# Optimization experiments

Hardware: AMD Instinct MI355X
Metric: run time of the kernel (lower is better)

The kernel has to match this reference:

```python
import jax, jax.numpy as jnp
import numpy as np

D_MODEL = 1024
N_HEADS = 16

def setup_inputs() -> dict:
    key = jax.random.key(0)
    k1, k2, k3, k4 = jax.random.split(key, 4)
    B, L, S = 4, 2048, 2048
    return {
        "queries": jax.random.normal(k1, (B, L, D_MODEL), dtype=jnp.float32),
        "keys": jax.random.normal(k2, (B, S, D_MODEL), dtype=jnp.float32),
        "values": jax.random.normal(k3, (B, S, D_MODEL), dtype=jnp.float32),
        "mask": jax.random.uniform(k4, (L, S), dtype=jnp.float32),
    }

def reference(queries, keys, values, mask):
    B, L, _ = queries.shape
    S = keys.shape[1]
    H = N_HEADS
    q = queries.reshape(B, L, H, -1)  # (B,L,H,E)
    k = keys.reshape(B, S, H, -1)     # (B,S,H,E)
    v = values.reshape(B, S, H, -1)   # (B,S,H,D)
    E = q.shape[-1]
    scale = 1.0 / jnp.sqrt(jnp.asarray(E, q.dtype))
    scores = jnp.einsum('blhe,bshe->bhls', q, k)  # (B,H,L,S)
    A = jax.nn.softmax(scale * scores, axis=-1)
    # post-softmax multiplicative mask, broadcast over (B,H)
    A = A * mask
    out = jnp.einsum('bhls,bshd->blhd', A, v)  # (B,L,H,D)
    # mix=True: transpose(2,1) then flatten -> reshape (B,H,L,D) contiguously to (B,L,H*D)
    out = jnp.transpose(out, (0, 2, 1, 3)).reshape(B, L, -1)
    return out
```

## Files before the change

kernel.cpp:

```cpp
#include <hip/hip_runtime.h>
#include <hip/hip_bf16.h>

#define NH 16
#define LQ 2048
#define SK 2048
#define QTILE 128
#define KVB 32
#define NSBLK (SK / KVB)
#define TILE_BYTES 8192
#define MTILE_BYTES 8192
#define KV_BYTES ((size_t)4 * NH * NSBLK * TILE_BYTES)
#define MASK_OFF KV_BYTES
#define WS_NEED (KV_BYTES + (size_t)16 * NSBLK * MTILE_BYTES)
#define KSTR 72

typedef __bf16 bf16_t;
typedef bf16_t bf16x8 __attribute__((ext_vector_type(8)));
typedef bf16_t bf16x4 __attribute__((ext_vector_type(4)));
typedef bf16_t bf16x2 __attribute__((ext_vector_type(2)));
typedef float f32x16 __attribute__((ext_vector_type(16)));
typedef float f32x4 __attribute__((ext_vector_type(4)));
typedef unsigned int uint2v __attribute__((ext_vector_type(2)));
typedef unsigned int uint4v __attribute__((ext_vector_type(4)));

union U4B8 { uint4v u; bf16x8 v; };

__device__ __forceinline__ bf16x8 cvt8v(f32x4 a, f32x4 b) {
  bf16x8 r;
  r[0]=(bf16_t)a[0]; r[1]=(bf16_t)a[1]; r[2]=(bf16_t)a[2]; r[3]=(bf16_t)a[3];
  r[4]=(bf16_t)b[0]; r[5]=(bf16_t)b[1]; r[6]=(bf16_t)b[2]; r[7]=(bf16_t)b[3];
  return r;
}
__device__ __forceinline__ unsigned pk2(float lo, float hi) {
  bf16x2 t; t[0] = (bf16_t)lo; t[1] = (bf16_t)hi;
  return __builtin_bit_cast(unsigned, t);
}
__device__ __forceinline__ void gll16(const void* g, void* l) {
  __builtin_amdgcn_global_load_lds(
      (const __attribute__((address_space(1))) unsigned int*)g,
      (__attribute__((address_space(3))) unsigned int*)l, 16, 0, 0);
}

__global__ __launch_bounds__(256) void repack_kv(const float* __restrict__ Kg,
                                                 const float* __restrict__ Vg,
                                                 unsigned char* __restrict__ ws)
{
  __shared__ __align__(16) unsigned short vlds[64 * 40];
  const int sblk = blockIdx.x, bh = blockIdx.y;
  const int b = bh >> 4, h = bh & 15;
  const int tid = threadIdx.x;
  const int row = tid >> 3;
  const int cq  = tid & 7;
  const int xr  = (row & 7) << 4;
  unsigned char* tile = ws + ((size_t)bh * NSBLK + sblk) * TILE_BYTES;

  {
    const float* kp = Kg + ((size_t)b * SK + sblk * KVB + row) * 1024 + h * 64 + cq * 8;
    f32x4 a = *(const f32x4*)kp;
    f32x4 b4 = *(const f32x4*)(kp + 4);
    *(bf16x8*)(tile + row * 128 + ((cq * 16) ^ xr)) = cvt8v(a, b4);
  }
  {
    const float* vp = Vg + ((size_t)b * SK + sblk * KVB + row) * 1024 + h * 64 + cq * 8;
    f32x4 a = *(const f32x4*)vp;
    f32x4 b4 = *(const f32x4*)(vp + 4);
    #pragma unroll
    for (int j = 0; j < 4; j++) {
      vlds[(cq * 8 + j) * 40 + row]     = __builtin_bit_cast(unsigned short, (bf16_t)a[j]);
      vlds[(cq * 8 + 4 + j) * 40 + row] = __builtin_bit_cast(unsigned short, (bf16_t)b4[j]);
    }
    __syncthreads();
    const int dp = row + 32 * (cq >> 2);
    const int kvc = cq & 3;
    bf16x8 r0 = *(const bf16x8*)&vlds[dp * 40 + kvc * 8];
    *(bf16x8*)(tile + 4096 + row * 128 + ((cq * 16) ^ xr)) = r0;
  }
}

__global__ __launch_bounds__(256) void repack_mask(const float* __restrict__ Mg,
                                                   unsigned char* __restrict__ mt)
{
  const int t = blockIdx.x, lt = blockIdx.y;
  const int tid = threadIdx.x;
  const int line = tid >> 2;
  const int xr   = (line & 7) << 4;
  unsigned char* tile = mt + ((size_t)lt * NSBLK + t) * MTILE_BYTES;
  #pragma unroll
  for (int cc = 0; cc < 2; cc++) {
    const int ch = (tid & 3) * 2 + cc;
    const int q  = lt * 128 + line + 64 * (ch >> 2);
    const int kv = t * KVB + (ch & 3) * 8;
    const float* src = Mg + (size_t)q * SK + kv;
    f32x4 a = *(const f32x4*)src;
    f32x4 b = *(const f32x4*)(src + 4);
    *(bf16x8*)(tile + line * 128 + ((ch * 16) ^ xr)) = cvt8v(a, b);
  }
}

#define PF2(T_, KBUF, MBUF)                                                      \
  {                                                                              \
    const unsigned char* sk_ = gsrc + (size_t)(T_) * TILE_BYTES;                 \
    unsigned char* lk_ = &(KBUF)[w * 1024];                                      \
    _Pragma("unroll")                                                            \
    for (int r_ = 0; r_ < 2; r_++) gll16(sk_ + r_ * 4096, lk_ + r_ * 4096);      \
    const unsigned char* sm_ = gmask + (size_t)(T_) * MTILE_BYTES;               \
    unsigned char* lm_ = &(MBUF)[w * 1024];                                      \
    _Pragma("unroll")                                                            \
    for (int r_ = 0; r_ < 2; r_++) gll16(sm_ + r_ * 4096, lm_ + r_ * 4096);      \
  }

#define TILE_STEP(KBUF, MBUF, KNXT, MNXT, T)                                     \
  {                                                                              \
    if ((T) + 1 < NSBLK) { PF2((T) + 1, KNXT, MNXT) }                            \
    f32x16 s_;                                                                   \
    _Pragma("unroll")                                                            \
    for (int m_ = 0; m_ < 16; m_++) s_[m_] = 0.f;                                \
    __builtin_amdgcn_s_setprio(1);                                               \
    _Pragma("unroll")                                                            \
    for (int ec_ = 0; ec_ < 4; ec_++) {                                          \
      bf16x8 kf_ = *(const bf16x8*)((KBUF) + q32 * 128 + ((ec_ * 32 + hi * 16) ^ xr)); \
      s_ = __builtin_amdgcn_mfma_f32_32x32x16_bf16(kf_, qf[ec_], s_, 0, 0, 0);   \
    }                                                                            \
    __builtin_amdgcn_s_setprio(0);                                               \
    float ts_ = 0.f;                                                             \
    _Pragma("unroll")                                                            \
    for (int m_ = 0; m_ < 16; m_++) { s_[m_] = exp2f(s_[m_]); ts_ += s_[m_]; }   \
    zloc += ts_;                                                                 \
    bf16x4 mk_[4];                                                               \
    _Pragma("unroll")                                                            \
    for (int u_ = 0; u_ < 4; u_++)                                               \
      mk_[u_] = *(const bf16x4*)((MBUF) + mboff +                                \
                   ((mhalf + u_ * 16 + hi * 8) ^ mxr));                          \
    _Pragma("unroll")                                                            \
    for (int m_ = 0; m_ < 16; m_++) s_[m_] *= (float)mk_[m_ >> 2][m_ & 3];       \
    bf16x8 pf_[2];                                                               \
    _Pragma("unroll")                                                            \
    for (int c_ = 0; c_ < 2; c_++) {                                             \
      unsigned a0_ = pk2(s_[8 * c_ + 0], s_[8 * c_ + 1]);                        \
      unsigned a1_ = pk2(s_[8 * c_ + 2], s_[8 * c_ + 3]);                        \
      unsigned b0_ = pk2(s_[8 * c_ + 4], s_[8 * c_ + 5]);                        \
      unsigned b1_ = pk2(s_[8 * c_ + 6], s_[8 * c_ + 7]);                        \
      uint2v r02_ = __builtin_amdgcn_permlane32_swap(a0_, b0_, false, false);    \
      uint2v r13_ = __builtin_amdgcn_permlane32_swap(a1_, b1_, false, false);    \
      U4B8 u_; u_.u = uint4v{r02_[0], r13_[0], r02_[1], r13_[1]};                \
      pf_[c_] = u_.v;                                                            \
    }                                                                            \
    __builtin_amdgcn_s_setprio(1);                                               \
    _Pragma("unroll")                                                            \
    for (int c_ = 0; c_ < 2; c_++) {                                             \
      bf16x8 vf0_ = *(const bf16x8*)((KBUF) + 4096 + q32 * 128 + ((c_ * 32 + hi * 16) ^ xr)); \
      acc0 = __builtin_amdgcn_mfma_f32_32x32x16_bf16(vf0_, pf_[c_], acc0, 0, 0, 0); \
      bf16x8 vf1_ = *(const bf16x8*)((KBUF) + 4096 + q32 * 128 + ((64 + c_ * 32 + hi * 16) ^ xr)); \
      acc1 = __builtin_amdgcn_mfma_f32_32x32x16_bf16(vf1_, pf_[c_], acc1, 0, 0, 0); \
    }                                                                            \
    __builtin_amdgcn_s_setprio(0);                                               \
    __syncthreads();                                                             \
  }

__global__ __launch_bounds__(256, 2)
void xattn2(const float* __restrict__ Qg, const unsigned char* __restrict__ WS,
            float* __restrict__ Og)
{
  __shared__ __align__(16) unsigned char kb0[TILE_BYTES];
  __shared__ __align__(16) unsigned char kb1[TILE_BYTES];
  __shared__ __align__(16) unsigned char mb0[MTILE_BYTES];
  __shared__ __align__(16) unsigned char mb1[MTILE_BYTES];

  const int f   = blockIdx.x;
  const int xcd = f & 7, ii = f >> 3;
  const int bh  = (xcd << 3) + (ii >> 4);
  const int lt  = ii & 15;
  const int b = bh >> 4, h = bh & 15;
  const int tid = threadIdx.x, w = tid >> 6, lane = tid & 63;
  const int q32 = lane & 31, hi = lane >> 5;
  const int qr0 = lt * QTILE + w * 32;
  const int xr  = (q32 & 7) << 4;
  const int mrow  = w * 32 + q32;
  const int mline = mrow & 63;
  const int mhalf = (mrow >> 6) << 6;
  const int mboff = mline * 128;
  const int mxr   = (mline & 7) << 4;

  const float qs = 0.125f * 1.44269504088896340736f;
  bf16x8 qf[4];
  {
    const float* qp = Qg + ((size_t)b * LQ + qr0 + q32) * 1024 + h * 64 + hi * 8;
    #pragma unroll
    for (int ec = 0; ec < 4; ec++) {
      f32x4 x = *(const f32x4*)(qp + ec * 16);
      f32x4 y = *(const f32x4*)(qp + ec * 16 + 4);
      #pragma unroll
      for (int j = 0; j < 4; j++) { x[j] *= qs; y[j] *= qs; }
      qf[ec] = cvt8v(x, y);
    }
  }

  f32x16 acc0, acc1;
  #pragma unroll
  for (int m = 0; m < 16; m++) { acc0[m] = 0.f; acc1[m] = 0.f; }
  float zloc = 0.f;

  const unsigned char* gsrc  = WS + (size_t)bh * NSBLK * TILE_BYTES + tid * 16;
  const unsigned char* gmask = WS + MASK_OFF + (size_t)lt * NSBLK * MTILE_BYTES + tid * 16;

  PF2(0, kb0, mb0)
  __syncthreads();

  #pragma unroll 1
  for (int tp = 0; tp < NSBLK / 2; ++tp) {
    TILE_STEP(kb0, mb0, kb1, mb1, 2 * tp)
    TILE_STEP(kb1, mb1, kb0, mb0, 2 * tp + 1)
  }

  {
    float zrun = zloc + __shfl_xor(zloc, 32);
    float inv = 1.0f / zrun;
    float* op = Og + ((size_t)bh * LQ + qr0 + q32) * 64 + hi * 4;
    #pragma unroll
    for (int mq = 0; mq < 4; mq++) {
      f32x4 o0, o1;
      #pragma unroll
      for (int r = 0; r < 4; r++) { o0[r] = acc0[4 * mq + r] * inv; o1[r] = acc1[4 * mq + r] * inv; }
      *(f32x4*)(op + mq * 8) = o0;
      *(f32x4*)(op + 32 + mq * 8) = o1;
    }
  }
}

__global__ __launch_bounds__(256, 2)
void xattn_fwd(const float* __restrict__ Qg, const float* __restrict__ Kg,
               const float* __restrict__ Vg, const float* __restrict__ Mg,
               float* __restrict__ Og)
{
  __shared__ __align__(16) unsigned short Kt[64 * KSTR];
  __shared__ __align__(16) unsigned short Vt[64 * KSTR];
  const int f   = blockIdx.x + blockIdx.y * gridDim.x;
  const int xcd = f & 7;
  const int ii  = f >> 3;
  const int bh  = (xcd << 3) + (ii >> 4);
  const int lt  = ii & 15;
  const int b = bh >> 4, h = bh & 15;
  const int tid  = threadIdx.x;
  const int w    = tid >> 6;
  const int lane = tid & 63;
  const int q32  = lane & 31;
  const int hi   = lane >> 5;
  const int qr0  = lt * QTILE + w * 32;
  const float qs = 0.125f * 1.44269504088896340736f;
  bf16x8 qf[4];
  {
    const float* qp = Qg + ((size_t)b * LQ + qr0 + q32) * 1024 + h * 64 + hi * 8;
    #pragma unroll
    for (int ec = 0; ec < 4; ec++) {
      f32x4 x = *(const f32x4*)(qp + ec * 16);
      f32x4 y = *(const f32x4*)(qp + ec * 16 + 4);
      #pragma unroll
      for (int j = 0; j < 4; j++) { x[j] *= qs; y[j] *= qs; }
      qf[ec] = cvt8v(x, y);
    }
  }
  f32x16 acc0, acc1;
  #pragma unroll
  for (int m = 0; m < 16; m++) { acc0[m] = 0.f; acc1[m] = 0.f; }
  float mrun = -1e30f, zrun = 0.f;
  const int kr = tid >> 2;
  const int kc = (tid & 3) << 4;
  const int vd = tid & 63;
  const int vk0 = w << 4;
  const float* kbase = Kg + (size_t)b * SK * 1024 + h * 64;
  const float* vbase = Vg + (size_t)b * SK * 1024 + h * 64;
  const float* mbase = Mg + (size_t)(qr0 + q32) * SK + hi * 4;
  f32x4 ka, kb, kc4, kd;
  float vr[16];
  {
    const float* kp = kbase + (size_t)kr * 1024 + kc;
    ka = *(const f32x4*)kp;        kb = *(const f32x4*)(kp + 4);
    kc4 = *(const f32x4*)(kp + 8); kd = *(const f32x4*)(kp + 12);
    const float* vp = vbase + (size_t)vk0 * 1024 + vd;
    #pragma unroll
    for (int j = 0; j < 16; j++) vr[j] = vp[(size_t)j * 1024];
  }
  for (int s0 = 0; s0 < SK; s0 += 64) {
    bf16x8 kcv0 = cvt8v(ka, kb), kcv1 = cvt8v(kc4, kd);
    bf16x8 vcv0, vcv1;
    #pragma unroll
    for (int j = 0; j < 8; j++) { vcv0[j] = (bf16_t)vr[j]; vcv1[j] = (bf16_t)vr[8 + j]; }
    __syncthreads();
    *(bf16x8*)&Kt[kr * KSTR + kc] = kcv0;
    *(bf16x8*)&Kt[kr * KSTR + kc + 8] = kcv1;
    *(bf16x8*)&Vt[vd * KSTR + vk0] = vcv0;
    *(bf16x8*)&Vt[vd * KSTR + vk0 + 8] = vcv1;
    __syncthreads();
    f32x4 mk[8];
    {
      const float* mp = mbase + s0;
      #pragma unroll
      for (int kvt = 0; kvt < 2; kvt++)
        #pragma unroll
        for (int mq = 0; mq < 4; mq++)
          mk[kvt * 4 + mq] = *(const f32x4*)(mp + kvt * 32 + mq * 8);
    }
    if (s0 + 64 < SK) {
      const float* kp = kbase + (size_t)(s0 + 64 + kr) * 1024 + kc;
      ka = *(const f32x4*)kp;        kb = *(const f32x4*)(kp + 4);
      kc4 = *(const f32x4*)(kp + 8); kd = *(const f32x4*)(kp + 12);
      const float* vp = vbase + (size_t)(s0 + 64 + vk0) * 1024 + vd;
      #pragma unroll
      for (int j = 0; j < 16; j++) vr[j] = vp[(size_t)j * 1024];
    }
    f32x16 sT[2];
    #pragma unroll
    for (int m = 0; m < 16; m++) { sT[0][m] = 0.f; sT[1][m] = 0.f; }
    #pragma unroll
    for (int ec = 0; ec < 4; ec++) {
      bf16x8 kf0 = *(const bf16x8*)&Kt[q32 * KSTR + ec * 16 + hi * 8];
      sT[0] = __builtin_amdgcn_mfma_f32_32x32x16_bf16(kf0, qf[ec], sT[0], 0, 0, 0);
      bf16x8 kf1 = *(const bf16x8*)&Kt[(32 + q32) * KSTR + ec * 16 + hi * 8];
      sT[1] = __builtin_amdgcn_mfma_f32_32x32x16_bf16(kf1, qf[ec], sT[1], 0, 0, 0);
    }
    float rmax = sT[0][0];
    #pragma unroll
    for (int m = 1; m < 16; m++) rmax = fmaxf(rmax, sT[0][m]);
    #pragma unroll
    for (int m = 0; m < 16; m++) rmax = fmaxf(rmax, sT[1][m]);
    rmax = fmaxf(rmax, __shfl_xor(rmax, 32));
    if (!__all(rmax <= mrun + 6.0f)) {
      float nm = fmaxf(mrun, rmax);
      float corr = exp2f(mrun - nm);
      mrun = nm; zrun *= corr;
      #pragma unroll
      for (int m = 0; m < 16; m++) { acc0[m] *= corr; acc1[m] *= corr; }
    }
    float rs = 0.f;
    #pragma unroll
    for (int kvt = 0; kvt < 2; kvt++)
      #pragma unroll
      for (int m = 0; m < 16; m++) { sT[kvt][m] = exp2f(sT[kvt][m] - mrun); rs += sT[kvt][m]; }
    rs += __shfl_xor(rs, 32);
    zrun += rs;
    #pragma unroll
    for (int kvt = 0; kvt < 2; kvt++)
      #pragma unroll
      for (int m = 0; m < 16; m++) sT[kvt][m] *= mk[kvt * 4 + (m >> 2)][m & 3];
    bf16x8 pf[4];
    #pragma unroll
    for (int kvt = 0; kvt < 2; kvt++) {
      #pragma unroll
      for (int c = 0; c < 2; c++) {
        unsigned a0 = pk2(sT[kvt][8 * c + 0], sT[kvt][8 * c + 1]);
        unsigned a1 = pk2(sT[kvt][8 * c + 2], sT[kvt][8 * c + 3]);
        unsigned b0 = pk2(sT[kvt][8 * c + 4], sT[kvt][8 * c + 5]);
        unsigned b1 = pk2(sT[kvt][8 * c + 6], sT[kvt][8 * c + 7]);
        uint2v r02 = __builtin_amdgcn_permlane32_swap(a0, b0, false, false);
        uint2v r13 = __builtin_amdgcn_permlane32_swap(a1, b1, false, false);
        U4B8 u; u.u = uint4v{r02[0], r13[0], r02[1], r13[1]};
        pf[kvt * 2 + c] = u.v;
      }
    }
    #pragma unroll
    for (int c = 0; c < 4; c++) {
      bf16x8 vf0 = *(const bf16x8*)&Vt[q32 * KSTR + c * 16 + hi * 8];
      acc0 = __builtin_amdgcn_mfma_f32_32x32x16_bf16(vf0, pf[c], acc0, 0, 0, 0);
      bf16x8 vf1 = *(const bf16x8*)&Vt[(32 + q32) * KSTR + c * 16 + hi * 8];
      acc1 = __builtin_amdgcn_mfma_f32_32x32x16_bf16(vf1, pf[c], acc1, 0, 0, 0);
    }
  }
  {
    float inv = 1.0f / zrun;
    float* op = Og + ((size_t)bh * LQ + qr0 + q32) * 64 + hi * 4;
    #pragma unroll
    for (int mq = 0; mq < 4; mq++) {
      f32x4 o0, o1;
      #pragma unroll
      for (int r = 0; r < 4; r++) { o0[r] = acc0[4 * mq + r] * inv; o1[r] = acc1[4 * mq + r] * inv; }
      *(f32x4*)(op + mq * 8) = o0;
      *(f32x4*)(op + 32 + mq * 8) = o1;
    }
  }
}

extern "C" void kernel_launch(void* const* d_in, const int* in_sizes, int n_in,
                              void* d_out, int out_size, void* d_ws, size_t ws_size,
                              hipStream_t stream) {
  const float* Qg = (const float*)d_in[0];
  const float* Kg = (const float*)d_in[1];
  const float* Vg = (const float*)d_in[2];
  const float* Mg = (const float*)d_in[3];
  float* Og = (float*)d_out;
  if (ws_size >= WS_NEED) {
    unsigned char* ws = (unsigned char*)d_ws;
    repack_kv<<<dim3(NSBLK, 4 * NH), 256, 0, stream>>>(Kg, Vg, ws);
    repack_mask<<<dim3(NSBLK, 16), 256, 0, stream>>>(Mg, ws + MASK_OFF);
    xattn2<<<LQ / QTILE * 4 * NH, 256, 0, stream>>>(Qg, ws, Og);
  } else {
    xattn_fwd<<<dim3(LQ / QTILE, 4 * NH), 256, 0, stream>>>(Qg, Kg, Vg, Mg, Og);
  }
}
```

Measured before the change: 148.1 us.

## Split KV range across two blocks per query tile and combine partial outputs

```diff
diff --git a/kernel.cpp b/kernel.cpp
--- a/kernel.cpp
+++ b/kernel.cpp
@@ -11,7 +11,14 @@
 #define MTILE_BYTES 8192
 #define KV_BYTES ((size_t)4 * NH * NSBLK * TILE_BYTES)
 #define MASK_OFF KV_BYTES
-#define WS_NEED (KV_BYTES + (size_t)16 * NSBLK * MTILE_BYTES)
+#define MASK_BYTES ((size_t)16 * NSBLK * MTILE_BYTES)
+#define O1_OFF (MASK_OFF + MASK_BYTES)
+#define O1_BYTES ((size_t)4 * NH * LQ * 64 * 4)
+#define Z0_OFF (O1_OFF + O1_BYTES)
+#define Z_BYTES ((size_t)4 * NH * LQ * 4)
+#define Z1_OFF (Z0_OFF + Z_BYTES)
+#define WS_NEED_SPLIT (Z1_OFF + Z_BYTES)
+#define WS_NEED (KV_BYTES + MASK_BYTES)
 #define KSTR 72
 
 typedef __bf16 bf16_t;
@@ -95,6 +102,161 @@
     f32x4 b = *(const f32x4*)(src + 4);
     *(bf16x8*)(tile + line * 128 + ((ch * 16) ^ xr)) = cvt8v(a, b);
   }
+}
+
+#define PFK(T_, KBUF)                                                            \
+  {                                                                              \
+    const unsigned char* sk_ = gsrc + (size_t)(T_) * TILE_BYTES;                 \
+    unsigned char* lk_ = &(KBUF)[w * 1024];                                      \
+    _Pragma("unroll")                                                            \
+    for (int r_ = 0; r_ < 2; r_++) gll16(sk_ + r_ * 4096, lk_ + r_ * 4096);      \
+  }
+
+#define MLOADR(T_, MKP)                                                          \
+  {                                                                              \
+    const unsigned char* mp_ = gmaskL + (size_t)(T_) * MTILE_BYTES;              \
+    _Pragma("unroll")                                                            \
+    for (int u_ = 0; u_ < 4; u_++)                                               \
+      MKP[u_] = *(const bf16x4*)(mp_ + mboff + ((mhalf + u_ * 16 + hi * 8) ^ mxr)); \
+  }
+
+#define SSTEP(KBUF, KNXT, MKCUR, MKNXT, T)                                       \
+  {                                                                              \
+    if ((T) + 1 < tend) { PFK((T) + 1, KNXT) MLOADR((T) + 1, MKNXT) }            \
+    f32x16 s_;                                                                   \
+    _Pragma("unroll")                                                            \
+    for (int m_ = 0; m_ < 16; m_++) s_[m_] = 0.f;                                \
+    __builtin_amdgcn_s_setprio(1);                                               \
+    _Pragma("unroll")                                                            \
+    for (int ec_ = 0; ec_ < 4; ec_++) {                                          \
+      bf16x8 kf_ = *(const bf16x8*)((KBUF) + q32 * 128 + ((ec_ * 32 + hi * 16) ^ xr)); \
+      s_ = __builtin_amdgcn_mfma_f32_32x32x16_bf16(kf_, qf[ec_], s_, 0, 0, 0);   \
+    }                                                                            \
+    __builtin_amdgcn_s_setprio(0);                                               \
+    float ts_ = 0.f;                                                             \
+    _Pragma("unroll")                                                            \
+    for (int m_ = 0; m_ < 16; m_++) { s_[m_] = exp2f(s_[m_]); ts_ += s_[m_]; }   \
+    zloc += ts_;                                                                 \
+    _Pragma("unroll")                                                            \
+    for (int m_ = 0; m_ < 16; m_++) s_[m_] *= (float)MKCUR[m_ >> 2][m_ & 3];     \
+    bf16x8 pf_[2];                                                               \
+    _Pragma("unroll")                                                            \
+    for (int c_ = 0; c_ < 2; c_++) {                                             \
+      unsigned a0_ = pk2(s_[8 * c_ + 0], s_[8 * c_ + 1]);                        \
+      unsigned a1_ = pk2(s_[8 * c_ + 2], s_[8 * c_ + 3]);                        \
+      unsigned b0_ = pk2(s_[8 * c_ + 4], s_[8 * c_ + 5]);                        \
+      unsigned b1_ = pk2(s_[8 * c_ + 6], s_[8 * c_ + 7]);                        \
+      uint2v r02_ = __builtin_amdgcn_permlane32_swap(a0_, b0_, false, false);    \
+      uint2v r13_ = __builtin_amdgcn_permlane32_swap(a1_, b1_, false, false);    \
+      U4B8 u_; u_.u = uint4v{r02_[0], r13_[0], r02_[1], r13_[1]};                \
+      pf_[c_] = u_.v;                                                            \
+    }                                                                            \
+    __builtin_amdgcn_s_setprio(1);                                               \
+    _Pragma("unroll")                                                            \
+    for (int c_ = 0; c_ < 2; c_++) {                                             \
+      bf16x8 vf0_ = *(const bf16x8*)((KBUF) + 4096 + q32 * 128 + ((c_ * 32 + hi * 16) ^ xr)); \
+      acc0 = __builtin_amdgcn_mfma_f32_32x32x16_bf16(vf0_, pf_[c_], acc0, 0, 0, 0); \
+      bf16x8 vf1_ = *(const bf16x8*)((KBUF) + 4096 + q32 * 128 + ((64 + c_ * 32 + hi * 16) ^ xr)); \
+      acc1 = __builtin_amdgcn_mfma_f32_32x32x16_bf16(vf1_, pf_[c_], acc1, 0, 0, 0); \
+    }                                                                            \
+    __builtin_amdgcn_s_setprio(0);                                               \
+    __syncthreads();                                                             \
+  }
+
+__global__ __launch_bounds__(256, 2)
+void xattn_split(const float* __restrict__ Qg, unsigned char* __restrict__ WS,
+                 float* __restrict__ Og)
+{
+  __shared__ __align__(16) unsigned char kb0[TILE_BYTES];
+  __shared__ __align__(16) unsigned char kb1[TILE_BYTES];
+
+  const int f   = blockIdx.x;
+  const int xcd = f & 7, ii = f >> 3;
+  const int bh  = (xcd << 3) + (ii >> 5);
+  const int r5  = ii & 31;
+  const int lt  = r5 >> 1;
+  const int half = r5 & 1;
+  const int b = bh >> 4, h = bh & 15;
+  const int tid = threadIdx.x, w = tid >> 6, lane = tid & 63;
+  const int q32 = lane & 31, hi = lane >> 5;
+  const int qr0 = lt * QTILE + w * 32;
+  const int xr  = (q32 & 7) << 4;
+  const int mrow  = w * 32 + q32;
+  const int mline = mrow & 63;
+  const int mhalf = (mrow >> 6) << 6;
+  const int mboff = mline * 128;
+  const int mxr   = (mline & 7) << 4;
+  const int tbase = half * (NSBLK / 2);
+  const int tend  = tbase + NSBLK / 2;
+
+  const float qs = 0.125f * 1.44269504088896340736f;
+  bf16x8 qf[4];
+  {
+    const float* qp = Qg + ((size_t)b * LQ + qr0 + q32) * 1024 + h * 64 + hi * 8;
+    #pragma unroll
+    for (int ec = 0; ec < 4; ec++) {
+      f32x4 x = *(const f32x4*)(qp + ec * 16);
+      f32x4 y = *(const f32x4*)(qp + ec * 16 + 4);
+      #pragma unroll
+      for (int j = 0; j < 4; j++) { x[j] *= qs; y[j] *= qs; }
+      qf[ec] = cvt8v(x, y);
+    }
+  }
+
+  f32x16 acc0, acc1;
+  #pragma unroll
+  for (int m = 0; m < 16; m++) { acc0[m] = 0.f; acc1[m] = 0.f; }
+  float zloc = 0.f;
+
+  const unsigned char* gsrc   = WS + (size_t)bh * NSBLK * TILE_BYTES + tid * 16;
+  const unsigned char* gmaskL = WS + MASK_OFF + (size_t)lt * NSBLK * MTILE_BYTES;
+
+  bf16x4 mkA[4], mkB[4];
+
+  PFK(tbase, kb0)
+  MLOADR(tbase, mkA)
+  __syncthreads();
+
+  #pragma unroll 1
+  for (int tp = 0; tp < NSBLK / 4; ++tp) {
+    SSTEP(kb0, kb1, mkA, mkB, tbase + 2 * tp)
+    SSTEP(kb1, kb0, mkB, mkA, tbase + 2 * tp + 1)
+  }
+
+  {
+    float zrun = zloc + __shfl_xor(zloc, 32);
+    float* obase = (half == 0)
+        ? (Og + ((size_t)bh * LQ + qr0 + q32) * 64 + hi * 4)
+        : ((float*)(WS + O1_OFF) + ((size_t)bh * LQ + qr0 + q32) * 64 + hi * 4);
+    #pragma unroll
+    for (int mq = 0; mq < 4; mq++) {
+      f32x4 o0, o1;
+      #pragma unroll
+      for (int r = 0; r < 4; r++) { o0[r] = acc0[4 * mq + r]; o1[r] = acc1[4 * mq + r]; }
+      *(f32x4*)(obase + mq * 8) = o0;
+      *(f32x4*)(obase + 32 + mq * 8) = o1;
+    }
+    if (hi == 0) {
+      float* zb = (float*)(WS + (half == 0 ? Z0_OFF : Z1_OFF));
+      zb[((size_t)bh << 11) + qr0 + q32] = zrun;
+    }
+  }
+}
+
+__global__ __launch_bounds__(256) void combine(float* __restrict__ Og,
+                                               const unsigned char* __restrict__ WS)
+{
+  const int i = blockIdx.x * 256 + threadIdx.x;
+  const int row = i >> 4;
+  const float* z0 = (const float*)(WS + Z0_OFF);
+  const float* z1 = (const float*)(WS + Z1_OFF);
+  const f32x4* O1 = (const f32x4*)(WS + O1_OFF);
+  float inv = 1.0f / (z0[row] + z1[row]);
+  f32x4 a = ((f32x4*)Og)[i];
+  f32x4 b = O1[i];
+  #pragma unroll
+  for (int j = 0; j < 4; j++) a[j] = (a[j] + b[j]) * inv;
+  ((f32x4*)Og)[i] = a;
 }
 
 #define PF2(T_, KBUF, MBUF)                                                      \
@@ -387,7 +549,13 @@
   const float* Vg = (const float*)d_in[2];
   const float* Mg = (const float*)d_in[3];
   float* Og = (float*)d_out;
-  if (ws_size >= WS_NEED) {
+  if (ws_size >= WS_NEED_SPLIT) {
+    unsigned char* ws = (unsigned char*)d_ws;
+    repack_kv<<<dim3(NSBLK, 4 * NH), 256, 0, stream>>>(Kg, Vg, ws);
+    repack_mask<<<dim3(NSBLK, 16), 256, 0, stream>>>(Mg, ws + MASK_OFF);
+    xattn_split<<<2 * (LQ / QTILE) * 4 * NH, 256, 0, stream>>>(Qg, ws, Og);
+    combine<<<(4 * NH * LQ * 64 / 4) / 256, 256, 0, stream>>>(Og, ws);
+  } else if (ws_size >= WS_NEED) {
     unsigned char* ws = (unsigned char*)d_ws;
     repack_kv<<<dim3(NSBLK, 4 * NH), 256, 0, stream>>>(Kg, Vg, ws);
     repack_mask<<<dim3(NSBLK, 16), 256, 0, stream>>>(Mg, ws + MASK_OFF);
```

New measurement: 169.1 us. 1.14x slower.
